# Optimization experiments

Hardware: AMD Instinct MI355X
Metric: run time of the kernel (lower is better)

## Reference

```python
import jax, jax.numpy as jnp
import numpy as np

ENERGY = 0.5  # target low-frequency energy ratio (init kwarg)
B, C, H, W = 8, 32, 512, 512


def setup_inputs() -> dict:
    key = jax.random.key(0)
    x = jax.random.normal(key, (B, C, H, W), dtype=jnp.float32)
    return {"x": x}


def reference(x) -> jnp.ndarray:
    b, c, h, w = x.shape
    crow, ccol = h // 2, w // 2

    f = jnp.fft.fft2(x)                       # [B,C,H,W] complex
    fshift = jnp.fft.fftshift(f, axes=(-2, -1))

    # Per-pixel minimal cutoff c such that pixel lies in the centered
    # square [crow-c:crow+c, ccol-c:ccol+c] (rows crow-c .. crow+c-1).
    ii = jnp.arange(h)
    jj = jnp.arange(w)
    c_row = jnp.maximum(crow - ii, ii - crow + 1)          # [H]
    c_col = jnp.maximum(ccol - jj, jj - ccol + 1)          # [W]
    c_needed = jnp.maximum(c_row[:, None], c_col[None, :])  # [H,W] int

    # Energy of channel 0 spectrum per batch element.
    e0 = jnp.abs(fshift[:, 0]) ** 2                         # [B,H,W]
    num_seg = int(max(crow, h - crow, ccol, w - ccol)) + 1
    seg = c_needed.reshape(-1)
    ring_energy = jax.vmap(
        lambda e: jax.ops.segment_sum(e.reshape(-1), seg, num_segments=num_seg)
    )(e0)                                                   # [B, num_seg]
    cum_energy = jnp.cumsum(ring_energy, axis=1)            # cum_energy[:, c] = low-freq energy at cutoff c
    total = cum_energy[:, -1]
    target = total * ENERGY

    # Search c in range(1, min(h,w)//2); first c with cum >= target, else 5.
    cmax = min(h, w) // 2
    cand = cum_energy[:, 1:cmax] >= target[:, None]          # [B, cmax-1]
    found = jnp.any(cand, axis=1)
    first = jnp.argmax(cand, axis=1) + 1                     # first satisfying cutoff
    cutoff = jnp.where(found, first, 5)                      # [B] int

    # Zero the centered square (same cutoff for all channels of a sample).
    keep = c_needed[None, :, :] > cutoff[:, None, None]      # [B,H,W] bool
    fshift = fshift * keep[:, None, :, :].astype(fshift.dtype)

    ishift = jnp.fft.ifftshift(fshift, axes=(-2, -1))
    return jnp.abs(jnp.fft.ifft2(ishift))
```

## Files before the change

kernel.cpp:

```cpp
#include <hip/hip_runtime.h>
#include <math.h>

#define FN 512
#define TPB 256
#define NIMG 256
#define NBATCH 8
#define NCH 32
#define NBINS 257
#define WACOLS 257
#define SPITCH 516

typedef unsigned long long ull;

__device__ __forceinline__ float2 cadd(float2 a, float2 b) { return make_float2(a.x + b.x, a.y + b.y); }
__device__ __forceinline__ float2 csub(float2 a, float2 b) { return make_float2(a.x - b.x, a.y - b.y); }
__device__ __forceinline__ float2 cmul(float2 a, float2 b) {
  return make_float2(fmaf(a.x, b.x, -a.y * b.y), fmaf(a.x, b.y, a.y * b.x));
}
template<bool INV>
__device__ __forceinline__ float2 cmul_s(float2 a, float2 w) {
  if (!INV) return make_float2(fmaf(a.x, w.x, -a.y * w.y), fmaf(a.x, w.y,  a.y * w.x));
  else      return make_float2(fmaf(a.x, w.x,  a.y * w.y), fmaf(a.y, w.x, -a.x * w.y));
}
__device__ __forceinline__ float2 cexpm(float ang) {
  float s, c;
  __sincosf(ang, &s, &c);
  return make_float2(c, s);
}
template<bool INV>
__device__ __forceinline__ float2 mulpmi(float2 a) {
  return INV ? make_float2(-a.y, a.x) : make_float2(a.y, -a.x);
}

template<bool INV>
__device__ __forceinline__ void dft8(float2 r[8]) {
  const float C = 0.70710678118654752440f;
  float2 t0 = cadd(r[0], r[4]), t1 = csub(r[0], r[4]);
  float2 t2 = cadd(r[2], r[6]), t3 = mulpmi<INV>(csub(r[2], r[6]));
  float2 E0 = cadd(t0, t2), E1 = cadd(t1, t3), E2 = csub(t0, t2), E3 = csub(t1, t3);
  float2 u0 = cadd(r[1], r[5]), u1 = csub(r[1], r[5]);
  float2 u2 = cadd(r[3], r[7]), u3 = mulpmi<INV>(csub(r[3], r[7]));
  float2 O0 = cadd(u0, u2), O1 = cadd(u1, u3), O2 = csub(u0, u2), O3 = csub(u1, u3);
  float2 O1w, O2w, O3w;
  if (!INV) {
    O1w = make_float2(C * (O1.x + O1.y), C * (O1.y - O1.x));
    O2w = make_float2(O2.y, -O2.x);
    O3w = make_float2(C * (O3.y - O3.x), -C * (O3.x + O3.y));
  } else {
    O1w = make_float2(C * (O1.x - O1.y), C * (O1.y + O1.x));
    O2w = make_float2(-O2.y, O2.x);
    O3w = make_float2(-C * (O3.x + O3.y), C * (O3.x - O3.y));
  }
  r[0] = cadd(E0, O0); r[1] = cadd(E1, O1w); r[2] = cadd(E2, O2w); r[3] = cadd(E3, O3w);
  r[4] = csub(E0, O0); r[5] = csub(E1, O1w); r[6] = csub(E2, O2w); r[7] = csub(E3, O3w);
}

__device__ __forceinline__ int swz(int q) {
  int b = (q >> 6) & 7;
  return q ^ b ^ ((b & 4) << 1);
}

#define TWOPI 6.2831853071795864769f

__device__ __forceinline__ void build_tw(int t, float2 tw512[7], float2 tw64[7]) {
  float2 w1 = cexpm(-TWOPI * (float)t * (1.0f / 512.0f));
  tw512[0] = w1;
  #pragma unroll
  for (int k = 1; k < 7; ++k) tw512[k] = cmul(tw512[k - 1], w1);
  float2 v1 = cexpm(-TWOPI * (float)(t & 7) * (1.0f / 64.0f));
  tw64[0] = v1;
  #pragma unroll
  for (int e = 1; e < 7; ++e) tw64[e] = cmul(tw64[e - 1], v1);
}

template<bool INV>
__device__ __forceinline__ void fft512_dif2(float2 rA[8], float2 rB[8],
                                            float2* __restrict__ LA, float2* __restrict__ LB,
                                            int t, const float2 tw512[7], const float2 tw64[7]) {
  dft8<INV>(rA);
  dft8<INV>(rB);
  #pragma unroll
  for (int k = 1; k < 8; ++k) {
    rA[k] = cmul_s<INV>(rA[k], tw512[k - 1]);
    rB[k] = cmul_s<INV>(rB[k], tw512[k - 1]);
  }
  #pragma unroll
  for (int k = 0; k < 8; ++k) { LA[swz(64 * k + t)] = rA[k]; LB[swz(64 * k + t)] = rB[k]; }
  const int base = 64 * (t >> 3) + (t & 7);
  #pragma unroll
  for (int d = 0; d < 8; ++d) rA[d] = LA[swz(base + 8 * d)];
  #pragma unroll
  for (int d = 0; d < 8; ++d) rB[d] = LB[swz(base + 8 * d)];
  dft8<INV>(rA);
  dft8<INV>(rB);
  #pragma unroll
  for (int e = 1; e < 8; ++e) {
    rA[e] = cmul_s<INV>(rA[e], tw64[e - 1]);
    rB[e] = cmul_s<INV>(rB[e], tw64[e - 1]);
  }
  #pragma unroll
  for (int e = 0; e < 8; ++e) { LA[swz(base + 8 * e)] = rA[e]; LB[swz(base + 8 * e)] = rB[e]; }
  #pragma unroll
  for (int m = 0; m < 8; ++m) rA[m] = LA[swz(8 * t + m)];
  #pragma unroll
  for (int m = 0; m < 8; ++m) rB[m] = LB[swz(8 * t + m)];
  dft8<INV>(rA);
  dft8<INV>(rB);
}

template<bool INV>
__device__ __forceinline__ void fft512_dit2(float2 rA[8], float2 rB[8],
                                            float2* __restrict__ LA, float2* __restrict__ LB,
                                            int t, const float2 tw64[7], float2 w0, float2 st) {
  dft8<INV>(rA);
  dft8<INV>(rB);
  #pragma unroll
  for (int c = 1; c < 8; ++c) {
    rA[c] = cmul_s<INV>(rA[c], tw64[c - 1]);
    rB[c] = cmul_s<INV>(rB[c], tw64[c - 1]);
  }
  #pragma unroll
  for (int c = 0; c < 8; ++c) { LA[swz(8 * t + c)] = rA[c]; LB[swz(8 * t + c)] = rB[c]; }
  const int base = 64 * (t >> 3) + (t & 7);
  #pragma unroll
  for (int e = 0; e < 8; ++e) rA[e] = LA[swz(base + 8 * e)];
  #pragma unroll
  for (int e = 0; e < 8; ++e) rB[e] = LB[swz(base + 8 * e)];
  dft8<INV>(rA);
  dft8<INV>(rB);
  {
    float2 w = w0;
    #pragma unroll
    for (int d = 0; d < 8; ++d) {
      rA[d] = cmul(rA[d], w);
      rB[d] = cmul(rB[d], w);
      w = cmul(w, st);
    }
  }
  #pragma unroll
  for (int d = 0; d < 8; ++d) { LA[swz(base + 8 * d)] = rA[d]; LB[swz(base + 8 * d)] = rB[d]; }
  #pragma unroll
  for (int j = 0; j < 8; ++j) rA[j] = LA[swz(64 * j + t)];
  #pragma unroll
  for (int j = 0; j < 8; ++j) rB[j] = LB[swz(64 * j + t)];
  dft8<INV>(rA);
  dft8<INV>(rB);
}

template<bool INV>
__device__ __forceinline__ void fft512_dif(float2 r[8], float2* __restrict__ L, int t,
                                           const float2 tw512[7], const float2 tw64[7]) {
  dft8<INV>(r);
  #pragma unroll
  for (int k = 1; k < 8; ++k) r[k] = cmul_s<INV>(r[k], tw512[k - 1]);
  #pragma unroll
  for (int k = 0; k < 8; ++k) L[swz(64 * k + t)] = r[k];
  const int base = 64 * (t >> 3) + (t & 7);
  #pragma unroll
  for (int d = 0; d < 8; ++d) r[d] = L[swz(base + 8 * d)];
  dft8<INV>(r);
  #pragma unroll
  for (int e = 1; e < 8; ++e) r[e] = cmul_s<INV>(r[e], tw64[e - 1]);
  #pragma unroll
  for (int e = 0; e < 8; ++e) L[swz(base + 8 * e)] = r[e];
  #pragma unroll
  for (int m = 0; m < 8; ++m) r[m] = L[swz(8 * t + m)];
  dft8<INV>(r);
}

__device__ __forceinline__ int ringc(int u) { return (u < 256) ? (u + 1) : (512 - u); }

__global__ __launch_bounds__(TPB, 4) void k_fwd_real(const float* __restrict__ x,
                                                     float2* __restrict__ W,
                                                     int img0, int img_stride) {
  __shared__ float2 stg[8][SPITCH];
  const int g = threadIdx.x >> 6, t = threadIdx.x & 63;
  const int li = blockIdx.x >> 5;
  const int R0 = (blockIdx.x & 31) * 16;
  const int img = img0 + li * img_stride;
  const float* __restrict__ base = x + (size_t)img * (FN * FN);
  float2 tw512[7], tw64[7];
  build_tw(t, tw512, tw64);
  {
    const float* __restrict__ raA = base + (size_t)(R0 + 2 * g) * FN;
    const float* __restrict__ rbA = raA + FN;
    const float* __restrict__ raB = base + (size_t)(R0 + 8 + 2 * g) * FN;
    const float* __restrict__ rbB = raB + FN;
    float2 rA[8], rB[8];
    #pragma unroll
    for (int j = 0; j < 8; ++j) {
      rA[j] = make_float2(raA[t + 64 * j], rbA[t + 64 * j]);
      rB[j] = make_float2(raB[t + 64 * j], rbB[t + 64 * j]);
    }
    fft512_dif2<false>(rA, rB, &stg[g][0], &stg[4 + g][0], t, tw512, tw64);
    #pragma unroll
    for (int f = 0; f < 8; ++f) {
      int p = 64 * f + 8 * (t & 7) + (t >> 3);
      stg[g][p] = rA[f];
      stg[4 + g][p] = rB[f];
    }
  }
  __syncthreads();
  float2* __restrict__ dst = W + (size_t)li * (WACOLS * FN);
  const int pr = threadIdx.x & 7;
  const int u0 = threadIdx.x >> 3;
  #pragma unroll
  for (int kk = 0; kk < 8; ++kk) {
    int u = u0 + 32 * kk;
    float2 Za = stg[pr][u];
    float2 Zb = stg[pr][(512 - u) & 511];
    float2 Fa = make_float2(0.5f * (Za.x + Zb.x), 0.5f * (Za.y - Zb.y));
    float2 Fb = make_float2(0.5f * (Za.y + Zb.y), 0.5f * (Zb.x - Za.x));
    float4* d4 = (float4*)(dst + (size_t)u * FN + R0 + 2 * pr);
    *d4 = make_float4(Fa.x, Fa.y, Fb.x, Fb.y);
  }
  if (threadIdx.x < 8) {
    float2 Z = stg[threadIdx.x][256];
    float4* d4 = (float4*)(dst + (size_t)256 * FN + R0 + 2 * threadIdx.x);
    *d4 = make_float4(Z.x, 0.f, Z.y, 0.f);
  }
}

__global__ __launch_bounds__(TPB) void k_ring(const float2* __restrict__ W1p, ull* __restrict__ bins) {
  __shared__ float2 ex[4][FN];
  __shared__ ull lbins[NBINS];
  const int g = threadIdx.x >> 6, t = threadIdx.x & 63;
  for (int i = threadIdx.x; i < NBINS; i += TPB) lbins[i] = 0;
  __syncthreads();
  const int li = blockIdx.x / 33;
  const int U0 = (blockIdx.x % 33) * 8;
  const float2* __restrict__ src = W1p + (size_t)li * (WACOLS * FN);
  float2 tw512[7], tw64[7];
  build_tw(t, tw512, tw64);
  #pragma unroll
  for (int s = 0; s < 2; ++s) {
    const int u = U0 + 4 * s + g;
    if (u > 256) continue;
    const float2* __restrict__ row = src + (size_t)u * FN;
    float2 r[8];
    #pragma unroll
    for (int j = 0; j < 8; ++j) r[j] = row[t + 64 * j];
    fft512_dif<false>(r, &ex[g][0], t, tw512, tw64);
    const int cu = ringc(u);
    const bool mir = (u >= 1 && u <= 255);
    const int cmu = mir ? ringc(512 - u) : 0;
    #pragma unroll
    for (int f = 0; f < 8; ++f) {
      int v = 64 * f + 8 * (t & 7) + (t >> 3);
      float e = fmaf(r[f].x, r[f].x, r[f].y * r[f].y);
      ull q = (ull)((double)e * 1048576.0);
      atomicAdd(&lbins[max(cu, ringc(v))], q);
      if (mir) atomicAdd(&lbins[max(cmu, ringc((512 - v) & 511))], q);
    }
  }
  __syncthreads();
  for (int i = threadIdx.x; i < NBINS; i += TPB)
    if (lbins[i]) atomicAdd(&bins[(size_t)li * NBINS + i], lbins[i]);
}

__global__ __launch_bounds__(64) void k_cutoff(const ull* __restrict__ bins, int* __restrict__ cut) {
  int b = threadIdx.x;
  if (b >= NBATCH) return;
  double tot = 0.0;
  for (int r = 0; r < NBINS; ++r) tot += (double)bins[b * NBINS + r];
  double target = 0.5 * tot;
  double cum = 0.0;
  int c = 5;
  bool found = false;
  for (int r = 0; r <= 255; ++r) {
    cum += (double)bins[b * NBINS + r];
    if (r >= 1 && !found && cum >= target) { c = r; found = true; }
  }
  cut[b] = c;
}

__global__ __launch_bounds__(TPB, 4) void k_mask(const float2* __restrict__ Wa, float2* __restrict__ Wb,
                                                 const int* __restrict__ cut, int img0) {
  __shared__ float2 stg[8][SPITCH];
  const int g = threadIdx.x >> 6, t = threadIdx.x & 63;
  const int li = blockIdx.x >> 6;
  const int U0 = (blockIdx.x & 63) * 8;
  const int cutoff = cut[(img0 + li) >> 5];
  bool anyLow = false;
  #pragma unroll
  for (int i = 0; i < 8; ++i) anyLow |= (ringc(U0 + i) <= cutoff);
  if (!anyLow) return;
  const float2* __restrict__ src = Wa + (size_t)li * (WACOLS * FN);
  float2 tw512[7], tw64[7];
  build_tw(t, tw512, tw64);
  const int tk = t >> 3, tc = t & 7;
  const float2 w0 = cexpm(TWOPI * (float)(tc * tk) * (1.0f / 512.0f));
  const float2 st = cexpm(TWOPI * (float)tk * (1.0f / 64.0f));
  const float sc = 1.0f / 512.0f;
  {
    const int uA = U0 + g, uB = U0 + 4 + g;
    if (ringc(uA) <= cutoff || ringc(uB) <= cutoff) {
      const bool mirA = (uA > 256), mirB = (uB > 256);
      const float2* __restrict__ rowA = src + (size_t)(mirA ? 512 - uA : uA) * FN;
      const float2* __restrict__ rowB = src + (size_t)(mirB ? 512 - uB : uB) * FN;
      float2 rA[8], rB[8];
      #pragma unroll
      for (int j = 0; j < 8; ++j) {
        rA[j] = rowA[t + 64 * j];
        rB[j] = rowB[t + 64 * j];
        if (mirA) rA[j].y = -rA[j].y;
        if (mirB) rB[j].y = -rB[j].y;
      }
      float2* LA = &stg[g][0];
      float2* LB = &stg[4 + g][0];
      fft512_dif2<false>(rA, rB, LA, LB, t, tw512, tw64);
      #pragma unroll
      for (int f = 0; f < 8; ++f) {
        int v = 64 * f + 8 * (t & 7) + (t >> 3);
        bool lo = (ringc(v) <= cutoff);
        rA[f] = lo ? make_float2(rA[f].x * sc, rA[f].y * sc) : make_float2(0.f, 0.f);
        rB[f] = lo ? make_float2(rB[f].x * sc, rB[f].y * sc) : make_float2(0.f, 0.f);
      }
      fft512_dit2<true>(rA, rB, LA, LB, t, tw64, w0, st);
      #pragma unroll
      for (int j = 0; j < 8; ++j) {
        stg[g][t + 64 * j] = rA[j];
        stg[4 + g][t + 64 * j] = rB[j];
      }
    }
  }
  __syncthreads();
  float2* __restrict__ dst = Wb + (size_t)li * (FN * FN);
  const int rl2 = threadIdx.x & 3;
  const int hg = threadIdx.x >> 2;
  #pragma unroll
  for (int kk = 0; kk < 8; ++kk) {
    int h = hg + 64 * kk;
    float2 a = stg[2 * rl2][h];
    float2 b = stg[2 * rl2 + 1][h];
    float4* d4 = (float4*)(dst + (size_t)h * FN + U0 + 2 * rl2);
    *d4 = make_float4(a.x, a.y, b.x, b.y);
  }
}

__global__ __launch_bounds__(TPB, 4) void k_inv_abs(const float2* __restrict__ Wb,
                                                    const float* __restrict__ x,
                                                    float* __restrict__ out,
                                                    const int* __restrict__ cut, int img0) {
  __shared__ float2 ex[8][FN];
  const int g = threadIdx.x >> 6, t = threadIdx.x & 63;
  const int li = blockIdx.x >> 6;
  const int H0 = (blockIdx.x & 63) * 8;
  const int img = img0 + li;
  const int cutoff = cut[img >> 5];
  const float2* __restrict__ src = Wb + (size_t)li * (FN * FN);
  const float* __restrict__ xbase = x + (size_t)img * (FN * FN);
  float* __restrict__ obase = out + (size_t)img * (FN * FN);
  float2 tw512[7], tw64[7];
  build_tw(t, tw512, tw64);
  const float sc = 1.0f / 512.0f;
  const int hA = H0 + g, hB = H0 + 4 + g;
  const float2* __restrict__ rowA = src + (size_t)hA * FN;
  const float2* __restrict__ rowB = src + (size_t)hB * FN;
  float2 rA[8], rB[8];
  #pragma unroll
  for (int j = 0; j < 8; ++j) {
    int u = t + 64 * j;
    bool lo = (ringc(u) <= cutoff);
    float2 vA = rowA[u];
    float2 vB = rowB[u];
    rA[j] = lo ? make_float2(vA.x * sc, vA.y * sc) : make_float2(0.f, 0.f);
    rB[j] = lo ? make_float2(vB.x * sc, vB.y * sc) : make_float2(0.f, 0.f);
  }
  fft512_dif2<true>(rA, rB, &ex[g][0], &ex[4 + g][0], t, tw512, tw64);
  const float* __restrict__ xrowA = xbase + (size_t)hA * FN;
  const float* __restrict__ xrowB = xbase + (size_t)hB * FN;
  float* __restrict__ orowA = obase + (size_t)hA * FN;
  float* __restrict__ orowB = obase + (size_t)hB * FN;
  #pragma unroll
  for (int f = 0; f < 8; ++f) {
    int p = 64 * f + 8 * (t & 7) + (t >> 3);
    float xa = xrowA[p];
    float xb = xrowB[p];
    float reA = xa - rA[f].x;
    float reB = xb - rB[f].x;
    orowA[p] = sqrtf(fmaf(reA, reA, rA[f].y * rA[f].y));
    orowB[p] = sqrtf(fmaf(reB, reB, rB[f].y * rB[f].y));
  }
}

extern "C" void kernel_launch(void* const* d_in, const int* in_sizes, int n_in,
                              void* d_out, int out_size, void* d_ws, size_t ws_size,
                              hipStream_t stream) {
  const float* x = (const float*)d_in[0];
  float* out = (float*)d_out;
  char* ws = (char*)d_ws;

  size_t off = 0;
  ull* bins = (ull*)(ws + off);
  off += ((size_t)NBATCH * NBINS * sizeof(ull) + 255) & ~(size_t)255;
  int* cut = (int*)(ws + off);
  off += 256;
  float2* W1p = (float2*)(ws + off);
  off += (size_t)NBATCH * WACOLS * FN * sizeof(float2);

  const size_t per_wa = (size_t)WACOLS * FN * sizeof(float2);
  const size_t per_wb = (size_t)FN * FN * sizeof(float2);
  size_t avail = (ws_size > off) ? (ws_size - off) : 0;
  int K = (int)(avail / (per_wa + per_wb));
  if (K > 32) K = 32;
  if (K < 1) K = 1;
  float2* WA = (float2*)(ws + off);
  float2* WB = (float2*)(ws + off + (size_t)K * per_wa);

  hipMemsetAsync(bins, 0, (size_t)NBATCH * NBINS * sizeof(ull), stream);

  hipLaunchKernelGGL(k_fwd_real, dim3(NBATCH * 32), dim3(TPB), 0, stream, x, W1p, 0, NCH);
  hipLaunchKernelGGL(k_ring,     dim3(NBATCH * 33), dim3(TPB), 0, stream, W1p, bins);
  hipLaunchKernelGGL(k_cutoff,   dim3(1),           dim3(64),  0, stream, bins, cut);

  for (int c0 = 0; c0 < NIMG; c0 += K) {
    int nk = (NIMG - c0 < K) ? (NIMG - c0) : K;
    hipLaunchKernelGGL(k_fwd_real, dim3(nk * 32), dim3(TPB), 0, stream, x, WA, c0, 1);
    hipLaunchKernelGGL(k_mask,     dim3(nk * 64), dim3(TPB), 0, stream, WA, WB, cut, c0);
    hipLaunchKernelGGL(k_inv_abs,  dim3(nk * 64), dim3(TPB), 0, stream, WB, x, out, cut, c0);
  }
}
```

Before: 580.3 us.

## Exploit Hermitian symmetry to halve column and row FFT work in masked inverse

The forward real FFT now writes only the half-spectrum columns up to the cutoff. The column pass processes only those half columns, packing two real-output rows into one complex inverse row FFT. Boundary terms that the half-spectrum packing misses (the cutoff column/row and its mirror) are captured into small side buffers. A new k_bvec kernel and per-row corrections in k_rows add them back. This cuts global traffic and FFT count for the intermediate buffer, but adds a serial O(cutoff) per-pixel-column sum kernel and more complex correction arithmetic that risks precision or edge-case errors.

Result: slower. 808.0 us (+39.2%).

```diff
diff --git a/kernel.cpp b/kernel.cpp
--- a/kernel.cpp
+++ b/kernel.cpp
@@ -8,6 +8,7 @@
 #define NCH 32
 #define NBINS 257
 #define WACOLS 257
+#define WBS 256
 #define SPITCH 516
 
 typedef unsigned long long ull;
@@ -172,12 +173,15 @@
 
 __global__ __launch_bounds__(TPB, 4) void k_fwd_real(const float* __restrict__ x,
                                                      float2* __restrict__ W,
-                                                     int img0, int img_stride) {
+                                                     int img0, int img_stride,
+                                                     const int* __restrict__ cut, int use_cut) {
   __shared__ float2 stg[8][SPITCH];
   const int g = threadIdx.x >> 6, t = threadIdx.x & 63;
   const int li = blockIdx.x >> 5;
   const int R0 = (blockIdx.x & 31) * 16;
   const int img = img0 + li * img_stride;
+  int ulim = 256;
+  if (use_cut) ulim = cut[img >> 5];
   const float* __restrict__ base = x + (size_t)img * (FN * FN);
   float2 tw512[7], tw64[7];
   build_tw(t, tw512, tw64);
@@ -207,14 +211,16 @@
   #pragma unroll
   for (int kk = 0; kk < 8; ++kk) {
     int u = u0 + 32 * kk;
-    float2 Za = stg[pr][u];
-    float2 Zb = stg[pr][(512 - u) & 511];
-    float2 Fa = make_float2(0.5f * (Za.x + Zb.x), 0.5f * (Za.y - Zb.y));
-    float2 Fb = make_float2(0.5f * (Za.y + Zb.y), 0.5f * (Zb.x - Za.x));
-    float4* d4 = (float4*)(dst + (size_t)u * FN + R0 + 2 * pr);
-    *d4 = make_float4(Fa.x, Fa.y, Fb.x, Fb.y);
-  }
-  if (threadIdx.x < 8) {
+    if (u <= ulim) {
+      float2 Za = stg[pr][u];
+      float2 Zb = stg[pr][(512 - u) & 511];
+      float2 Fa = make_float2(0.5f * (Za.x + Zb.x), 0.5f * (Za.y - Zb.y));
+      float2 Fb = make_float2(0.5f * (Za.y + Zb.y), 0.5f * (Zb.x - Za.x));
+      float4* d4 = (float4*)(dst + (size_t)u * FN + R0 + 2 * pr);
+      *d4 = make_float4(Fa.x, Fa.y, Fb.x, Fb.y);
+    }
+  }
+  if (!use_cut && threadIdx.x < 8) {
     float2 Z = stg[threadIdx.x][256];
     float4* d4 = (float4*)(dst + (size_t)256 * FN + R0 + 2 * threadIdx.x);
     *d4 = make_float4(Z.x, 0.f, Z.y, 0.f);
@@ -274,58 +280,70 @@
   cut[b] = c;
 }
 
-__global__ __launch_bounds__(TPB, 4) void k_mask(const float2* __restrict__ Wa, float2* __restrict__ Wb,
+__global__ __launch_bounds__(TPB, 4) void k_cols(const float2* __restrict__ Wa,
+                                                 float2* __restrict__ Wb,
+                                                 float2* __restrict__ Abuf,
+                                                 float2* __restrict__ Bv,
+                                                 float2* __restrict__ Fc,
+                                                 float2* __restrict__ c4raw,
                                                  const int* __restrict__ cut, int img0) {
   __shared__ float2 stg[8][SPITCH];
   const int g = threadIdx.x >> 6, t = threadIdx.x & 63;
-  const int li = blockIdx.x >> 6;
-  const int U0 = (blockIdx.x & 63) * 8;
+  const int li = blockIdx.x >> 5;
+  const int U0 = (blockIdx.x & 31) * 8;
   const int cutoff = cut[(img0 + li) >> 5];
-  bool anyLow = false;
-  #pragma unroll
-  for (int i = 0; i < 8; ++i) anyLow |= (ringc(U0 + i) <= cutoff);
-  if (!anyLow) return;
+  const int NC = 512 - cutoff;
+  if (U0 > cutoff) return;
   const float2* __restrict__ src = Wa + (size_t)li * (WACOLS * FN);
   float2 tw512[7], tw64[7];
   build_tw(t, tw512, tw64);
   const int tk = t >> 3, tc = t & 7;
-  const float2 w0 = cexpm(TWOPI * (float)(tc * tk) * (1.0f / 512.0f));
-  const float2 st = cexpm(TWOPI * (float)tk * (1.0f / 64.0f));
+  const float2 w0d = cexpm(TWOPI * (float)(tc * tk) * (1.0f / 512.0f));
+  const float2 std = cexpm(TWOPI * (float)tk * (1.0f / 64.0f));
   const float sc = 1.0f / 512.0f;
-  {
-    const int uA = U0 + g, uB = U0 + 4 + g;
-    if (ringc(uA) <= cutoff || ringc(uB) <= cutoff) {
-      const bool mirA = (uA > 256), mirB = (uB > 256);
-      const float2* __restrict__ rowA = src + (size_t)(mirA ? 512 - uA : uA) * FN;
-      const float2* __restrict__ rowB = src + (size_t)(mirB ? 512 - uB : uB) * FN;
-      float2 rA[8], rB[8];
-      #pragma unroll
-      for (int j = 0; j < 8; ++j) {
-        rA[j] = rowA[t + 64 * j];
-        rB[j] = rowB[t + 64 * j];
-        if (mirA) rA[j].y = -rA[j].y;
-        if (mirB) rB[j].y = -rB[j].y;
-      }
-      float2* LA = &stg[g][0];
-      float2* LB = &stg[4 + g][0];
-      fft512_dif2<false>(rA, rB, LA, LB, t, tw512, tw64);
-      #pragma unroll
-      for (int f = 0; f < 8; ++f) {
-        int v = 64 * f + 8 * (t & 7) + (t >> 3);
-        bool lo = (ringc(v) <= cutoff);
-        rA[f] = lo ? make_float2(rA[f].x * sc, rA[f].y * sc) : make_float2(0.f, 0.f);
-        rB[f] = lo ? make_float2(rB[f].x * sc, rB[f].y * sc) : make_float2(0.f, 0.f);
-      }
-      fft512_dit2<true>(rA, rB, LA, LB, t, tw64, w0, st);
-      #pragma unroll
-      for (int j = 0; j < 8; ++j) {
-        stg[g][t + 64 * j] = rA[j];
-        stg[4 + g][t + 64 * j] = rB[j];
-      }
-    }
+  const int uA = U0 + g, uB = U0 + 4 + g;
+  const float2* __restrict__ rowA = src + (size_t)uA * FN;
+  const float2* __restrict__ rowB = src + (size_t)uB * FN;
+  float2 rA[8], rB[8];
+  #pragma unroll
+  for (int j = 0; j < 8; ++j) { rA[j] = rowA[t + 64 * j]; rB[j] = rowB[t + 64 * j]; }
+  float2* LA = &stg[g][0];
+  float2* LB = &stg[4 + g][0];
+  fft512_dif2<false>(rA, rB, LA, LB, t, tw512, tw64);
+  const int vt = 8 * tc + tk;
+  #pragma unroll
+  for (int f = 0; f < 8; ++f) {
+    int v = 64 * f + vt;
+    if (v == cutoff) {
+      if (uA < cutoff) Fc[li * 256 + uA] = rA[f];
+      else if (uA == cutoff) c4raw[li] = rA[f];
+      if (uB < cutoff) Fc[li * 256 + uB] = rB[f];
+      else if (uB == cutoff) c4raw[li] = rB[f];
+    }
+    if (v == NC) {
+      if (uA < cutoff) Bv[li * 256 + uA] = rA[f];
+      if (uB < cutoff) Bv[li * 256 + uB] = rB[f];
+    }
+  }
+  #pragma unroll
+  for (int f = 0; f < 8; ++f) {
+    int v = 64 * f + vt;
+    bool lo = (v < cutoff) || (v > NC);
+    rA[f] = lo ? make_float2(rA[f].x * sc, rA[f].y * sc) : make_float2(0.f, 0.f);
+    rB[f] = lo ? make_float2(rB[f].x * sc, rB[f].y * sc) : make_float2(0.f, 0.f);
+  }
+  fft512_dit2<true>(rA, rB, LA, LB, t, tw64, w0d, std);
+  const bool aA = (uA == cutoff), aB = (uB == cutoff);
+  #pragma unroll
+  for (int j = 0; j < 8; ++j) {
+    int h = t + 64 * j;
+    stg[g][h] = rA[j];
+    stg[4 + g][h] = rB[j];
+    if (aA) Abuf[li * 512 + h] = rA[j];
+    if (aB) Abuf[li * 512 + h] = rB[j];
   }
   __syncthreads();
-  float2* __restrict__ dst = Wb + (size_t)li * (FN * FN);
+  float2* __restrict__ dst = Wb + (size_t)li * (512 * WBS);
   const int rl2 = threadIdx.x & 3;
   const int hg = threadIdx.x >> 2;
   #pragma unroll
@@ -333,54 +351,127 @@
     int h = hg + 64 * kk;
     float2 a = stg[2 * rl2][h];
     float2 b = stg[2 * rl2 + 1][h];
-    float4* d4 = (float4*)(dst + (size_t)h * FN + U0 + 2 * rl2);
+    float4* d4 = (float4*)(dst + (size_t)h * WBS + U0 + 2 * rl2);
     *d4 = make_float4(a.x, a.y, b.x, b.y);
   }
 }
 
-__global__ __launch_bounds__(TPB, 4) void k_inv_abs(const float2* __restrict__ Wb,
-                                                    const float* __restrict__ x,
-                                                    float* __restrict__ out,
-                                                    const int* __restrict__ cut, int img0) {
+__global__ __launch_bounds__(TPB) void k_bvec(const float2* __restrict__ Bv,
+                                              const float2* __restrict__ Fc,
+                                              float2* __restrict__ bvec,
+                                              const int* __restrict__ cut, int img0) {
+  const int li = blockIdx.x;
+  const int cutoff = cut[(img0 + li) >> 5];
+  const float2* __restrict__ bp = Bv + li * 256;
+  const float2* __restrict__ fp = Fc + li * 256;
+  const float s2 = 1.0f / (512.0f * 512.0f);
+  for (int w = threadIdx.x; w < 512; w += TPB) {
+    float2 sA = cexpm(TWOPI * (float)w * (1.0f / 512.0f));
+    float2 sB = make_float2(sA.x, -sA.y);
+    float2 pA = make_float2(1.f, 0.f), pB = make_float2(1.f, 0.f);
+    float2 acc = make_float2(0.f, 0.f);
+    for (int u = 0; u < cutoff; ++u) {
+      acc = cadd(acc, cmul(bp[u], pA));
+      if (u >= 1) {
+        float2 F = fp[u];
+        acc = cadd(acc, cmul(make_float2(F.x, -F.y), pB));
+      }
+      pA = cmul(pA, sA);
+      pB = cmul(pB, sB);
+    }
+    bvec[li * 512 + w] = make_float2(acc.x * s2, acc.y * s2);
+  }
+}
+
+__global__ __launch_bounds__(TPB, 3) void k_rows(const float2* __restrict__ Wb,
+                                                 const float2* __restrict__ Abuf,
+                                                 const float2* __restrict__ bvec,
+                                                 const float2* __restrict__ c4raw,
+                                                 const float* __restrict__ x,
+                                                 float* __restrict__ out,
+                                                 const int* __restrict__ cut, int img0) {
   __shared__ float2 ex[8][FN];
   const int g = threadIdx.x >> 6, t = threadIdx.x & 63;
-  const int li = blockIdx.x >> 6;
-  const int H0 = (blockIdx.x & 63) * 8;
+  const int li = blockIdx.x >> 5;
+  const int H0 = (blockIdx.x & 31) * 16;
   const int img = img0 + li;
   const int cutoff = cut[img >> 5];
-  const float2* __restrict__ src = Wb + (size_t)li * (FN * FN);
+  const int NC = 512 - cutoff;
+  const float2* __restrict__ wbase = Wb + (size_t)li * (512 * WBS);
   const float* __restrict__ xbase = x + (size_t)img * (FN * FN);
   float* __restrict__ obase = out + (size_t)img * (FN * FN);
   float2 tw512[7], tw64[7];
   build_tw(t, tw512, tw64);
   const float sc = 1.0f / 512.0f;
-  const int hA = H0 + g, hB = H0 + 4 + g;
-  const float2* __restrict__ rowA = src + (size_t)hA * FN;
-  const float2* __restrict__ rowB = src + (size_t)hB * FN;
+  const int h1 = H0 + 2 * g, h2 = h1 + 1, h3 = h1 + 8, h4 = h2 + 8;
+  const float2* __restrict__ r1 = wbase + (size_t)h1 * WBS;
+  const float2* __restrict__ r2 = wbase + (size_t)h2 * WBS;
+  const float2* __restrict__ r3 = wbase + (size_t)h3 * WBS;
+  const float2* __restrict__ r4 = wbase + (size_t)h4 * WBS;
   float2 rA[8], rB[8];
   #pragma unroll
   for (int j = 0; j < 8; ++j) {
     int u = t + 64 * j;
-    bool lo = (ringc(u) <= cutoff);
-    float2 vA = rowA[u];
-    float2 vB = rowB[u];
-    rA[j] = lo ? make_float2(vA.x * sc, vA.y * sc) : make_float2(0.f, 0.f);
-    rB[j] = lo ? make_float2(vB.x * sc, vB.y * sc) : make_float2(0.f, 0.f);
+    float2 zA, zB;
+    if (u < cutoff) {
+      float2 m1 = r1[u], m2 = r2[u], m3 = r3[u], m4 = r4[u];
+      zA = make_float2(m1.x - m2.y, m1.y + m2.x);
+      zB = make_float2(m3.x - m4.y, m3.y + m4.x);
+    } else if (u > NC) {
+      int um = 512 - u;
+      float2 m1 = r1[um], m2 = r2[um], m3 = r3[um], m4 = r4[um];
+      zA = make_float2(m1.x + m2.y, -m1.y + m2.x);
+      zB = make_float2(m3.x + m4.y, -m3.y + m4.x);
+    } else {
+      zA = make_float2(0.f, 0.f);
+      zB = make_float2(0.f, 0.f);
+    }
+    rA[j] = make_float2(zA.x * sc, zA.y * sc);
+    rB[j] = make_float2(zB.x * sc, zB.y * sc);
   }
   fft512_dif2<true>(rA, rB, &ex[g][0], &ex[4 + g][0], t, tw512, tw64);
-  const float* __restrict__ xrowA = xbase + (size_t)hA * FN;
-  const float* __restrict__ xrowB = xbase + (size_t)hB * FN;
-  float* __restrict__ orowA = obase + (size_t)hA * FN;
-  float* __restrict__ orowB = obase + (size_t)hB * FN;
+  const float s2 = sc * sc;
+  float2 cv = c4raw[li];
+  const float2 c4 = make_float2(cv.x * s2, -cv.y * s2);
+  float2 wv1 = cexpm(TWOPI * (float)((NC * h1) & 511) * (1.0f / 512.0f));
+  float2 wv2 = cexpm(TWOPI * (float)((NC * h2) & 511) * (1.0f / 512.0f));
+  float2 wv3 = cexpm(TWOPI * (float)((NC * h3) & 511) * (1.0f / 512.0f));
+  float2 wv4 = cexpm(TWOPI * (float)((NC * h4) & 511) * (1.0f / 512.0f));
+  float2 A1 = Abuf[li * 512 + h1], A2 = Abuf[li * 512 + h2];
+  float2 A3 = Abuf[li * 512 + h3], A4 = Abuf[li * 512 + h4];
+  float2 A1p = cadd(make_float2(A1.x * sc, -A1.y * sc), cmul(c4, wv1));
+  float2 A2p = cadd(make_float2(A2.x * sc, -A2.y * sc), cmul(c4, wv2));
+  float2 A3p = cadd(make_float2(A3.x * sc, -A3.y * sc), cmul(c4, wv3));
+  float2 A4p = cadd(make_float2(A4.x * sc, -A4.y * sc), cmul(c4, wv4));
+  const int w0i = 8 * (t & 7) + (t >> 3);
+  float2 ph = cexpm(TWOPI * (float)((NC * w0i) & 511) * (1.0f / 512.0f));
+  const float2 s64 = cexpm(TWOPI * (float)((64 * (NC & 7)) & 511) * (1.0f / 512.0f));
+  const float* __restrict__ x1 = xbase + (size_t)h1 * FN;
+  const float* __restrict__ x2 = xbase + (size_t)h2 * FN;
+  const float* __restrict__ x3 = xbase + (size_t)h3 * FN;
+  const float* __restrict__ x4 = xbase + (size_t)h4 * FN;
+  float* __restrict__ o1 = obase + (size_t)h1 * FN;
+  float* __restrict__ o2 = obase + (size_t)h2 * FN;
+  float* __restrict__ o3 = obase + (size_t)h3 * FN;
+  float* __restrict__ o4 = obase + (size_t)h4 * FN;
+  const float2* __restrict__ bp = bvec + li * 512;
   #pragma unroll
   for (int f = 0; f < 8; ++f) {
-    int p = 64 * f + 8 * (t & 7) + (t >> 3);
-    float xa = xrowA[p];
-    float xb = xrowB[p];
-    float reA = xa - rA[f].x;
-    float reB = xb - rB[f].x;
-    orowA[p] = sqrtf(fmaf(reA, reA, rA[f].y * rA[f].y));
-    orowB[p] = sqrtf(fmaf(reB, reB, rB[f].y * rB[f].y));
+    int p = 64 * f + w0i;
+    float2 bv = bp[p];
+    float2 d1 = cadd(cmul(ph, A1p), cmul(wv1, bv));
+    float2 d2 = cadd(cmul(ph, A2p), cmul(wv2, bv));
+    float2 d3 = cadd(cmul(ph, A3p), cmul(wv3, bv));
+    float2 d4 = cadd(cmul(ph, A4p), cmul(wv4, bv));
+    float e1 = x1[p] - rA[f].x - d1.x;
+    float e2 = x2[p] - rA[f].y - d2.x;
+    float e3 = x3[p] - rB[f].x - d3.x;
+    float e4 = x4[p] - rB[f].y - d4.x;
+    o1[p] = sqrtf(fmaf(e1, e1, d1.y * d1.y));
+    o2[p] = sqrtf(fmaf(e2, e2, d2.y * d2.y));
+    o3[p] = sqrtf(fmaf(e3, e3, d3.y * d3.y));
+    o4[p] = sqrtf(fmaf(e4, e4, d4.y * d4.y));
+    ph = cmul(ph, s64);
   }
 }
 
@@ -400,24 +491,31 @@
   off += (size_t)NBATCH * WACOLS * FN * sizeof(float2);
 
   const size_t per_wa = (size_t)WACOLS * FN * sizeof(float2);
-  const size_t per_wb = (size_t)FN * FN * sizeof(float2);
+  const size_t per_wb = (size_t)512 * WBS * sizeof(float2);
+  const size_t per_side = (size_t)(512 + 512 + 256 + 256 + 8) * sizeof(float2);
   size_t avail = (ws_size > off) ? (ws_size - off) : 0;
-  int K = (int)(avail / (per_wa + per_wb));
+  int K = (int)(avail / (per_wa + per_wb + per_side));
   if (K > 32) K = 32;
   if (K < 1) K = 1;
-  float2* WA = (float2*)(ws + off);
-  float2* WB = (float2*)(ws + off + (size_t)K * per_wa);
+  float2* WA = (float2*)(ws + off);               off += (size_t)K * per_wa;
+  float2* WB = (float2*)(ws + off);               off += (size_t)K * per_wb;
+  float2* Abuf = (float2*)(ws + off);             off += (size_t)K * 512 * sizeof(float2);
+  float2* bvec = (float2*)(ws + off);             off += (size_t)K * 512 * sizeof(float2);
+  float2* Bv = (float2*)(ws + off);               off += (size_t)K * 256 * sizeof(float2);
+  float2* Fc = (float2*)(ws + off);               off += (size_t)K * 256 * sizeof(float2);
+  float2* c4raw = (float2*)(ws + off);            off += (size_t)K * 8 * sizeof(float2);
 
   hipMemsetAsync(bins, 0, (size_t)NBATCH * NBINS * sizeof(ull), stream);
 
-  hipLaunchKernelGGL(k_fwd_real, dim3(NBATCH * 32), dim3(TPB), 0, stream, x, W1p, 0, NCH);
+  hipLaunchKernelGGL(k_fwd_real, dim3(NBATCH * 32), dim3(TPB), 0, stream, x, W1p, 0, NCH, cut, 0);
   hipLaunchKernelGGL(k_ring,     dim3(NBATCH * 33), dim3(TPB), 0, stream, W1p, bins);
   hipLaunchKernelGGL(k_cutoff,   dim3(1),           dim3(64),  0, stream, bins, cut);
 
   for (int c0 = 0; c0 < NIMG; c0 += K) {
     int nk = (NIMG - c0 < K) ? (NIMG - c0) : K;
-    hipLaunchKernelGGL(k_fwd_real, dim3(nk * 32), dim3(TPB), 0, stream, x, WA, c0, 1);
-    hipLaunchKernelGGL(k_mask,     dim3(nk * 64), dim3(TPB), 0, stream, WA, WB, cut, c0);
-    hipLaunchKernelGGL(k_inv_abs,  dim3(nk * 64), dim3(TPB), 0, stream, WB, x, out, cut, c0);
-  }
-}
+    hipLaunchKernelGGL(k_fwd_real, dim3(nk * 32), dim3(TPB), 0, stream, x, WA, c0, 1, cut, 1);
+    hipLaunchKernelGGL(k_cols,     dim3(nk * 32), dim3(TPB), 0, stream, WA, WB, Abuf, Bv, Fc, c4raw, cut, c0);
+    hipLaunchKernelGGL(k_bvec,     dim3(nk),      dim3(TPB), 0, stream, Bv, Fc, bvec, cut, c0);
+    hipLaunchKernelGGL(k_rows,     dim3(nk * 32), dim3(TPB), 0, stream, WB, Abuf, bvec, c4raw, x, out, cut, c0);
+  }
+}
```
